# Kernel tuning notes

Measured on AMD Instinct MI355X. Metric: run time of the kernel, lower is better.

Reference implementation:

```python
import math
import jax, jax.numpy as jnp
import numpy as np

B, S, D, H = 1, 4096, 1024, 16
HD = D // H


def setup_inputs() -> dict:
    key = jax.random.key(0)
    ks = jax.random.split(key, 11)
    s = 0.02
    inp = {
        "q": jax.random.normal(ks[0], (B, S, D), jnp.float32),
        "k": jax.random.normal(ks[1], (B, S, D), jnp.float32),
        "v": jax.random.normal(ks[2], (B, S, D), jnp.float32),
        # causal boolean mask, broadcastable over [B, H, S, S]
        "mask": jnp.tril(jnp.ones((S, S), jnp.bool_))[None, None],
        "Wq": jax.random.normal(ks[3], (D, D), jnp.float32) * s,
        "bq": jnp.zeros((D,), jnp.float32),
        "Wk": jax.random.normal(ks[4], (D, D), jnp.float32) * s,
        "bk": jnp.zeros((D,), jnp.float32),
        "Wv": jax.random.normal(ks[5], (D, D), jnp.float32) * s,
        "bv": jnp.zeros((D,), jnp.float32),
        "Wo": jax.random.normal(ks[6], (D, D), jnp.float32) * s,
        "bo": jnp.zeros((D,), jnp.float32),
    }
    return inp


def reference(q, k, v, mask, Wq, bq, Wk, bk, Wv, bv, Wo, bo):
    # projections (torch Linear: x @ W.T + b; here W is stored already transposed)
    qp = (q @ Wq + bq).reshape(B, S, H, HD)
    kp = (k @ Wk + bk).reshape(B, S, H, HD)
    vp = (v @ Wv + bv).reshape(B, S, H, HD)
    # scores: [B, H, S, S]
    scores = jnp.einsum("bqhd,bkhd->bhqk", qp, kp) / math.sqrt(HD)
    scores = jnp.where(mask, scores, -jnp.inf)
    attn = jax.nn.softmax(scores, axis=-1)
    # context: [B, H, S, HD] -> [B, S, D]
    ctx = jnp.einsum("bhqk,bkhd->bqhd", attn, vp).reshape(B, S, D)
    return ctx @ Wo + bo
```

## Files before the change

### kernel.cpp

```cpp
#include <hip/hip_runtime.h>
#include <hip/hip_bf16.h>


#define S_LEN 4096
#define D_DIM 1024
#define NHEAD 16
#define HDIM  64

typedef __hip_bfloat16 bf16;
typedef __attribute__((ext_vector_type(8))) short bf16x8v;
typedef __attribute__((ext_vector_type(4))) float f32x4;

#define MFMA16(a, b, c) __builtin_amdgcn_mfma_f32_16x16x32_bf16((a), (b), (c), 0, 0, 0)

__device__ __forceinline__ void async_cp16(const void* g, void* l) {
    __builtin_amdgcn_global_load_lds(
        (const __attribute__((address_space(1))) unsigned int*)g,
        (__attribute__((address_space(3))) unsigned int*)l, 16, 0, 0);
}

__global__ __launch_bounds__(256) void cvt_bf16_k(
    const float* __restrict__ x0, const float* __restrict__ x1,
    const float* __restrict__ x2,
    bf16* __restrict__ y0, bf16* __restrict__ y1, bf16* __restrict__ y2)
{
    const float* x = (blockIdx.z == 0) ? x0 : (blockIdx.z == 1) ? x1 : x2;
    bf16*       y = (blockIdx.z == 0) ? y0 : (blockIdx.z == 1) ? y1 : y2;
    const size_t i = ((size_t)blockIdx.x * 256 + threadIdx.x);
    const float4 v = ((const float4*)x)[i];
    union { bf16 h[4]; short4 s; } u;
    u.h[0] = __float2bfloat16(v.x);
    u.h[1] = __float2bfloat16(v.y);
    u.h[2] = __float2bfloat16(v.z);
    u.h[3] = __float2bfloat16(v.w);
    ((short4*)y)[i] = u.s;
}

__global__ __launch_bounds__(256) void transpose_cvt_k(
    const float* __restrict__ W0, const float* __restrict__ W1,
    const float* __restrict__ W2, const float* __restrict__ W3,
    bf16* __restrict__ T0, bf16* __restrict__ T1,
    bf16* __restrict__ T2, bf16* __restrict__ T3)
{
    const float* W = (blockIdx.z == 0) ? W0 : (blockIdx.z == 1) ? W1
                   : (blockIdx.z == 2) ? W2 : W3;
    bf16*       Wt = (blockIdx.z == 0) ? T0 : (blockIdx.z == 1) ? T1
                   : (blockIdx.z == 2) ? T2 : T3;
    __shared__ float t[32][33];
    const int bx = blockIdx.x << 5, by = blockIdx.y << 5;
    const int tx = threadIdx.x & 31, ty = threadIdx.x >> 5;
#pragma unroll
    for (int i = 0; i < 32; i += 8)
        t[ty + i][tx] = W[(size_t)(by + ty + i) * D_DIM + bx + tx];
    __syncthreads();
#pragma unroll
    for (int i = 0; i < 32; i += 8)
        Wt[(size_t)(bx + ty + i) * D_DIM + by + tx] = __float2bfloat16(t[tx][ty + i]);
}

struct GemmJob {
    const bf16* A; const bf16* Wt; const float* bias; void* out;
    int mode; float scale;
};

__global__ __launch_bounds__(256) void gemm_k(GemmJob j0, GemmJob j1, GemmJob j2)
{
    const GemmJob j = (blockIdx.z == 0) ? j0 : (blockIdx.z == 1) ? j1 : j2;
    const int K = D_DIM;
    const int bn = blockIdx.x << 6;
    const int bm = blockIdx.y << 7;
    const int tid = threadIdx.x;
    const int w = tid >> 6, lane = tid & 63;
    const int col = lane & 15, g = lane >> 4;
    const int wr = (w >> 1) << 6, wc = (w & 1) << 5;

    __shared__ bf16 As[128 * 64];
    __shared__ bf16 Bs[64 * 64];

    f32x4 acc[4][2];
#pragma unroll
    for (int i = 0; i < 4; ++i)
#pragma unroll
        for (int jj = 0; jj < 2; ++jj) acc[i][jj] = (f32x4){0.f, 0.f, 0.f, 0.f};

    for (int kb = 0; kb < K; kb += 64) {
        __syncthreads();
#pragma unroll
        for (int e = 0; e < 4; ++e) {
            const int lin = (e << 8) + tid;
            const int row = lin >> 3, kc = lin & 7;
            async_cp16(j.A + (size_t)(bm + row) * K + kb + (kc << 3), &As[lin << 3]);
        }
#pragma unroll
        for (int e = 0; e < 2; ++e) {
            const int lin = (e << 8) + tid;
            const int row = lin >> 3, kc = lin & 7;
            async_cp16(j.Wt + (size_t)(bn + row) * K + kb + (kc << 3), &Bs[lin << 3]);
        }
        __syncthreads();

#pragma unroll
        for (int s = 0; s < 2; ++s) {
            bf16x8v af[4], bfv[2];
#pragma unroll
            for (int i = 0; i < 4; ++i)
                af[i] = *(const bf16x8v*)&As[((wr + (i << 4) + col) << 6) + (s << 5) + (g << 3)];
#pragma unroll
            for (int jj = 0; jj < 2; ++jj)
                bfv[jj] = *(const bf16x8v*)&Bs[((wc + (jj << 4) + col) << 6) + (s << 5) + (g << 3)];
#pragma unroll
            for (int i = 0; i < 4; ++i)
#pragma unroll
                for (int jj = 0; jj < 2; ++jj)
                    acc[i][jj] = MFMA16(af[i], bfv[jj], acc[i][jj]);
        }
    }

#pragma unroll
    for (int i = 0; i < 4; ++i)
#pragma unroll
    for (int jj = 0; jj < 2; ++jj)
#pragma unroll
    for (int reg = 0; reg < 4; ++reg) {
        const int row = bm + wr + (i << 4) + (g << 2) + reg;
        const int cg  = bn + wc + (jj << 4) + col;
        const float vv = (acc[i][jj][reg] + j.bias[cg]) * j.scale;
        if (j.mode == 0)
            ((bf16*)j.out)[(((size_t)(cg >> 6)) * S_LEN + row) * HDIM + (cg & 63)] =
                __float2bfloat16(vv);
        else if (j.mode == 2)
            ((bf16*)j.out)[((size_t)(cg >> 6) * HDIM + (cg & 63)) * S_LEN + row] =
                __float2bfloat16(vv);
        else
            ((float*)j.out)[(size_t)row * D_DIM + cg] = vv;
    }
}

__global__ __launch_bounds__(256) void attn_mfma_k(
    const bf16* __restrict__ Qp, const bf16* __restrict__ Kp,
    const bf16* __restrict__ Vt, bf16* __restrict__ ctx)
{
    __shared__ bf16 Ks[4096];
    __shared__ bf16 Vs[4096];
    __shared__ bf16 Ps[4][1024];

    const int bid = blockIdx.x;
    const int qb  = 63 - (bid >> 4);
    const int h   = bid & 15;
    const int q0  = qb << 6;
    const int tid = threadIdx.x, w = tid >> 6, lane = tid & 63;
    const int col = lane & 15, g = lane >> 4;

    const bf16* Kh = Kp + (size_t)h * S_LEN * HDIM;
    const bf16* Vh = Vt + (size_t)h * HDIM * S_LEN;

    const size_t qrow_base = ((size_t)h * S_LEN + q0 + (w << 4) + col) * HDIM + (g << 3);
    const bf16x8v qf0 = *(const bf16x8v*)(Qp + qrow_base);
    const bf16x8v qf1 = *(const bf16x8v*)(Qp + qrow_base + 32);

    const int sig_r = (col >> 2) | (((col & 3) ^ (g & 1)) << 2);
    const int pr0 = (((g) << 4) | sig_r) << 3;
    const int pr1 = (((4 + g) << 4) | sig_r) << 3;
    int pw[4][4];
#pragma unroll
    for (int t = 0; t < 4; ++t) {
        const int Gw = (t << 1) + (col >> 3);
#pragma unroll
        for (int reg = 0; reg < 4; ++reg) {
            const int sig = g | (((reg ^ (Gw & 1)) & 3) << 2);
            pw[t][reg] = (((Gw << 4) | sig) << 3) + (col & 7);
        }
    }

    float pl[4] = {0.f, 0.f, 0.f, 0.f};
    f32x4 acco[4];
#pragma unroll
    for (int t = 0; t < 4; ++t) acco[t] = (f32x4){0.f, 0.f, 0.f, 0.f};

    const int nkb = qb + 1;
    for (int kb = 0; kb < nkb; ++kb) {
        const int kk0 = kb << 6;
        __syncthreads();
#pragma unroll
        for (int e = 0; e < 2; ++e) {
            const int lin = (e << 8) + tid;
            const int t = lin >> 7, G = (lin >> 4) & 7, c = lin & 15;
            async_cp16(Kh + (size_t)(kk0 + (t << 4) + c) * HDIM + (G << 3),
                       &Ks[lin << 3]);
            async_cp16(Vh + (size_t)((t << 4) + c) * S_LEN + kk0 + (G << 3),
                       &Vs[lin << 3]);
        }
        __syncthreads();

        f32x4 sa[4];
#pragma unroll
        for (int t = 0; t < 4; ++t) sa[t] = (f32x4){0.f, 0.f, 0.f, 0.f};
#pragma unroll
        for (int t = 0; t < 4; ++t) {
            sa[t] = MFMA16(qf0, *(const bf16x8v*)&Ks[((t << 7) + (g << 4) + col) << 3], sa[t]);
            sa[t] = MFMA16(qf1, *(const bf16x8v*)&Ks[((t << 7) + 64 + (g << 4) + col) << 3], sa[t]);
        }

        const bool lastt = (kb == nkb - 1);
#pragma unroll
        for (int t = 0; t < 4; ++t) {
#pragma unroll
            for (int reg = 0; reg < 4; ++reg) {
                float p;
                if (lastt && (kk0 + (t << 4) + col > q0 + (w << 4) + (g << 2) + reg))
                    p = 0.f;
                else
                    p = __expf(sa[t][reg]);
                pl[reg] += p;
                Ps[w][pw[t][reg]] = __float2bfloat16(p);
            }
        }

        const bf16x8v pf0 = *(const bf16x8v*)&Ps[w][pr0];
        const bf16x8v pf1 = *(const bf16x8v*)&Ps[w][pr1];
#pragma unroll
        for (int t = 0; t < 4; ++t) {
            acco[t] = MFMA16(pf0, *(const bf16x8v*)&Vs[((t << 7) + (g << 4) + col) << 3], acco[t]);
            acco[t] = MFMA16(pf1, *(const bf16x8v*)&Vs[((t << 7) + 64 + (g << 4) + col) << 3], acco[t]);
        }
    }

    float lrow[4];
#pragma unroll
    for (int reg = 0; reg < 4; ++reg) {
        float l = pl[reg];
        l += __shfl_xor(l, 1);
        l += __shfl_xor(l, 2);
        l += __shfl_xor(l, 4);
        l += __shfl_xor(l, 8);
        lrow[reg] = l;
    }

#pragma unroll
    for (int t = 0; t < 4; ++t)
#pragma unroll
        for (int reg = 0; reg < 4; ++reg) {
            const int row = q0 + (w << 4) + (g << 2) + reg;
            ctx[(size_t)row * D_DIM + h * HDIM + (t << 4) + col] =
                __float2bfloat16(acco[t][reg] / lrow[reg]);
        }
}

extern "C" void kernel_launch(void* const* d_in, const int* in_sizes, int n_in,
                              void* d_out, int out_size, void* d_ws, size_t ws_size,
                              hipStream_t stream)
{
    const float* q  = (const float*)d_in[0];
    const float* k  = (const float*)d_in[1];
    const float* v  = (const float*)d_in[2];
    const float* Wq = (const float*)d_in[4];
    const float* bq = (const float*)d_in[5];
    const float* Wk = (const float*)d_in[6];
    const float* bk = (const float*)d_in[7];
    const float* Wv = (const float*)d_in[8];
    const float* bv = (const float*)d_in[9];
    const float* Wo = (const float*)d_in[10];
    const float* bo = (const float*)d_in[11];

    const size_t PE  = (size_t)S_LEN * D_DIM;
    const size_t WTE = (size_t)D_DIM * D_DIM;

    const dim3 tg(32, 32, 4);
    const dim3 gg(D_DIM / 64, S_LEN / 128, 1);
    const dim3 gg3(D_DIM / 64, S_LEN / 128, 3);
    const dim3 cg((unsigned)(PE / 1024), 1, 3);

    if (ws_size >= (size_t)64 * 1024 * 1024) {
        bf16* Qb = (bf16*)d_ws;
        bf16* Kb = Qb + PE;
        bf16* Vb = Kb + PE;
        bf16* Qp = Vb + PE;
        bf16* Kp = Qp + PE;
        bf16* Vt = Kp + PE;
        bf16* Wtq = Vt + PE;
        bf16* Wtk = Wtq + WTE;
        bf16* Wtv = Wtk + WTE;
        bf16* Wto = Wtv + WTE;
        bf16* ctx = Qb;

        transpose_cvt_k<<<tg, 256, 0, stream>>>(Wq, Wk, Wv, Wo, Wtq, Wtk, Wtv, Wto);
        cvt_bf16_k<<<cg, 256, 0, stream>>>(q, k, v, Qb, Kb, Vb);

        GemmJob jq{Qb, Wtq, bq, Qp, 0, 0.125f};
        GemmJob jk{Kb, Wtk, bk, Kp, 0, 1.0f};
        GemmJob jv{Vb, Wtv, bv, Vt, 2, 1.0f};
        gemm_k<<<gg3, 256, 0, stream>>>(jq, jk, jv);

        attn_mfma_k<<<dim3(1024), 256, 0, stream>>>(Qp, Kp, Vt, ctx);

        GemmJob jo{ctx, Wto, bo, d_out, 1, 1.0f};
        gemm_k<<<gg, 256, 0, stream>>>(jo, jo, jo);
    } else {
        bf16* X  = (bf16*)d_ws;
        bf16* Qp = X + PE;
        bf16* Kp = Qp + PE;
        bf16* Vt = Kp + PE;
        bf16* Wtq = Vt + PE;
        bf16* Wtk = Wtq + WTE;
        bf16* Wtv = Wtk + WTE;
        bf16* Wto = Wtv + WTE;

        transpose_cvt_k<<<tg, 256, 0, stream>>>(Wq, Wk, Wv, Wo, Wtq, Wtk, Wtv, Wto);

        const dim3 cg1((unsigned)(PE / 1024), 1, 1);
        cvt_bf16_k<<<cg1, 256, 0, stream>>>(q, q, q, X, X, X);
        GemmJob jq{X, Wtq, bq, Qp, 0, 0.125f};
        gemm_k<<<gg, 256, 0, stream>>>(jq, jq, jq);
        cvt_bf16_k<<<cg1, 256, 0, stream>>>(k, k, k, X, X, X);
        GemmJob jk{X, Wtk, bk, Kp, 0, 1.0f};
        gemm_k<<<gg, 256, 0, stream>>>(jk, jk, jk);
        cvt_bf16_k<<<cg1, 256, 0, stream>>>(v, v, v, X, X, X);
        GemmJob jv{X, Wtv, bv, Vt, 2, 1.0f};
        gemm_k<<<gg, 256, 0, stream>>>(jv, jv, jv);

        attn_mfma_k<<<dim3(1024), 256, 0, stream>>>(Qp, Kp, Vt, X);

        GemmJob jo{X, Wto, bo, d_out, 1, 1.0f};
        gemm_k<<<gg, 256, 0, stream>>>(jo, jo, jo);
    }
}
```

Baseline: 324.3 us.

## Restructure attention: 128-row query tiles, register P, register-prefetched K/V, XOR-swizzled LDS

The attention kernel now handles 128 query rows per block (two 16-row tiles per wave), so each K/V tile staged in shared memory is reused twice as often, and the grid shrinks to 512 blocks. It computes S transposed so the exp'd probabilities can be packed straight into MFMA operand registers, removing the per-wave shared-memory P round trip. Q is pre-scaled by log2(e) so exp2 can replace expf. The V projection output is written in a permuted row order to match the new P register layout, and the next K/V tile is prefetched into registers while the current one is computed. The GEMM shared-memory tiles also get an XOR swizzle to cut bank conflicts; in exchange there are more registers per thread, fewer blocks, and a tightly coupled layout between the GEMM and attention kernels.

After: 328.9 us. Within noise of the previous version (+1.4%).

```diff
diff --git a/kernel.cpp b/kernel.cpp
--- a/kernel.cpp
+++ b/kernel.cpp
@@ -12,11 +12,16 @@
 typedef __attribute__((ext_vector_type(4))) float f32x4;
 
 #define MFMA16(a, b, c) __builtin_amdgcn_mfma_f32_16x16x32_bf16((a), (b), (c), 0, 0, 0)
+#define LOG2E 1.44269504088896340736f
 
 __device__ __forceinline__ void async_cp16(const void* g, void* l) {
     __builtin_amdgcn_global_load_lds(
         (const __attribute__((address_space(1))) unsigned int*)g,
         (__attribute__((address_space(3))) unsigned int*)l, 16, 0, 0);
+}
+
+__device__ __forceinline__ short bf_bits(float x) {
+    union { bf16 h; short s; } u; u.h = __float2bfloat16(x); return u.s;
 }
 
 __global__ __launch_bounds__(256) void cvt_bf16_k(
@@ -88,14 +93,16 @@
 #pragma unroll
         for (int e = 0; e < 4; ++e) {
             const int lin = (e << 8) + tid;
-            const int row = lin >> 3, kc = lin & 7;
-            async_cp16(j.A + (size_t)(bm + row) * K + kb + (kc << 3), &As[lin << 3]);
+            const int row = lin >> 3, kcs = lin & 7;
+            const int kcg = kcs ^ (row & 7);
+            async_cp16(j.A + (size_t)(bm + row) * K + kb + (kcg << 3), &As[lin << 3]);
         }
 #pragma unroll
         for (int e = 0; e < 2; ++e) {
             const int lin = (e << 8) + tid;
-            const int row = lin >> 3, kc = lin & 7;
-            async_cp16(j.Wt + (size_t)(bn + row) * K + kb + (kc << 3), &Bs[lin << 3]);
+            const int row = lin >> 3, kcs = lin & 7;
+            const int kcg = kcs ^ (row & 7);
+            async_cp16(j.Wt + (size_t)(bn + row) * K + kb + (kcg << 3), &Bs[lin << 3]);
         }
         __syncthreads();
 
@@ -103,11 +110,15 @@
         for (int s = 0; s < 2; ++s) {
             bf16x8v af[4], bfv[2];
 #pragma unroll
-            for (int i = 0; i < 4; ++i)
-                af[i] = *(const bf16x8v*)&As[((wr + (i << 4) + col) << 6) + (s << 5) + (g << 3)];
-#pragma unroll
-            for (int jj = 0; jj < 2; ++jj)
-                bfv[jj] = *(const bf16x8v*)&Bs[((wc + (jj << 4) + col) << 6) + (s << 5) + (g << 3)];
+            for (int i = 0; i < 4; ++i) {
+                const int row = wr + (i << 4) + col;
+                af[i] = *(const bf16x8v*)&As[((row << 3) + (((s << 2) + g) ^ (row & 7))) << 3];
+            }
+#pragma unroll
+            for (int jj = 0; jj < 2; ++jj) {
+                const int row = wc + (jj << 4) + col;
+                bfv[jj] = *(const bf16x8v*)&Bs[((row << 3) + (((s << 2) + g) ^ (row & 7))) << 3];
+            }
 #pragma unroll
             for (int i = 0; i < 4; ++i)
 #pragma unroll
@@ -128,122 +139,172 @@
         if (j.mode == 0)
             ((bf16*)j.out)[(((size_t)(cg >> 6)) * S_LEN + row) * HDIM + (cg & 63)] =
                 __float2bfloat16(vv);
-        else if (j.mode == 2)
-            ((bf16*)j.out)[((size_t)(cg >> 6) * HDIM + (cg & 63)) * S_LEN + row] =
+        else if (j.mode == 2) {
+            const int lr = row & 63;
+            const int prow = (row & ~63) | (lr & 32)
+                           | (((lr & 15) >> 2) << 3)
+                           | ((lr & 3) + (((lr >> 4) & 1) << 2));
+            ((bf16*)j.out)[((size_t)(cg >> 6) * HDIM + (cg & 63)) * S_LEN + prow] =
                 __float2bfloat16(vv);
-        else
+        } else
             ((float*)j.out)[(size_t)row * D_DIM + cg] = vv;
     }
 }
 
 __global__ __launch_bounds__(256) void attn_mfma_k(
     const bf16* __restrict__ Qp, const bf16* __restrict__ Kp,
-    const bf16* __restrict__ Vt, bf16* __restrict__ ctx)
+    const bf16* __restrict__ Vtm, bf16* __restrict__ ctx)
 {
     __shared__ bf16 Ks[4096];
     __shared__ bf16 Vs[4096];
-    __shared__ bf16 Ps[4][1024];
 
     const int bid = blockIdx.x;
-    const int qb  = 63 - (bid >> 4);
+    const int qb  = 31 - (bid >> 4);
     const int h   = bid & 15;
-    const int q0  = qb << 6;
+    const int q0  = qb << 7;
+    const int nkb = (qb << 1) + 2;
     const int tid = threadIdx.x, w = tid >> 6, lane = tid & 63;
     const int col = lane & 15, g = lane >> 4;
 
-    const bf16* Kh = Kp + (size_t)h * S_LEN * HDIM;
-    const bf16* Vh = Vt + (size_t)h * HDIM * S_LEN;
-
-    const size_t qrow_base = ((size_t)h * S_LEN + q0 + (w << 4) + col) * HDIM + (g << 3);
-    const bf16x8v qf0 = *(const bf16x8v*)(Qp + qrow_base);
-    const bf16x8v qf1 = *(const bf16x8v*)(Qp + qrow_base + 32);
-
-    const int sig_r = (col >> 2) | (((col & 3) ^ (g & 1)) << 2);
-    const int pr0 = (((g) << 4) | sig_r) << 3;
-    const int pr1 = (((4 + g) << 4) | sig_r) << 3;
-    int pw[4][4];
-#pragma unroll
-    for (int t = 0; t < 4; ++t) {
-        const int Gw = (t << 1) + (col >> 3);
+    const bf16* Kh = Kp  + (size_t)h * S_LEN * HDIM;
+    const bf16* Vh = Vtm + (size_t)h * HDIM * S_LEN;
+
+    bf16x8v qf[2][2];
+#pragma unroll
+    for (int u = 0; u < 2; ++u) {
+        const size_t qrb = ((size_t)h * S_LEN + q0 + (w << 5) + (u << 4) + col) * HDIM + (g << 3);
+        qf[u][0] = *(const bf16x8v*)(Qp + qrb);
+        qf[u][1] = *(const bf16x8v*)(Qp + qrb + 32);
+    }
+
+    const int L0 = tid, L1 = 256 + tid;
+    const int k0r = L0 >> 3, k0G = L0 & 7;
+    const int k1r = L1 >> 3, k1G = L1 & 7;
+    const int sl0 = ((k0r >> 4) << 7) + (k0G << 4) + ((k0r & 15) ^ k0G);
+    const int sl1 = ((k1r >> 4) << 7) + (k1G << 4) + ((k1r & 15) ^ k1G);
+    const size_t v0base = (size_t)k0r * S_LEN + (k0G << 3);
+    const size_t v1base = (size_t)k1r * S_LEN + (k1G << 3);
+
+    float pl[2] = {0.f, 0.f};
+    f32x4 acco[2][4];
+#pragma unroll
+    for (int u = 0; u < 2; ++u)
+#pragma unroll
+        for (int t = 0; t < 4; ++t) acco[u][t] = (f32x4){0.f, 0.f, 0.f, 0.f};
+
+    {
+        bf16x8v ka = *(const bf16x8v*)(Kh + ((size_t)L0 << 3));
+        bf16x8v kb_ = *(const bf16x8v*)(Kh + ((size_t)L1 << 3));
+        bf16x8v va = *(const bf16x8v*)(Vh + v0base);
+        bf16x8v vb = *(const bf16x8v*)(Vh + v1base);
+        *(bf16x8v*)&Ks[sl0 << 3] = ka;
+        *(bf16x8v*)&Ks[sl1 << 3] = kb_;
+        *(bf16x8v*)&Vs[sl0 << 3] = va;
+        *(bf16x8v*)&Vs[sl1 << 3] = vb;
+    }
+    __syncthreads();
+
+    for (int kb = 0; kb < nkb; ++kb) {
+        bf16x8v kn0, kn1, vn0, vn1;
+        const bool more = (kb + 1 < nkb);
+        if (more) {
+            const size_t kbase = (size_t)(kb + 1) << 12;
+            kn0 = *(const bf16x8v*)(Kh + kbase + ((size_t)L0 << 3));
+            kn1 = *(const bf16x8v*)(Kh + kbase + ((size_t)L1 << 3));
+            const int koff = (kb + 1) << 6;
+            vn0 = *(const bf16x8v*)(Vh + v0base + koff);
+            vn1 = *(const bf16x8v*)(Vh + v1base + koff);
+        }
+
+        f32x4 sa[2][4];
+#pragma unroll
+        for (int u = 0; u < 2; ++u)
+#pragma unroll
+            for (int t = 0; t < 4; ++t) sa[u][t] = (f32x4){0.f, 0.f, 0.f, 0.f};
+#pragma unroll
+        for (int t = 0; t < 4; ++t) {
+            const int G0 = g, G1 = 4 + g;
+            const bf16x8v kf0 = *(const bf16x8v*)&Ks[(((t << 7) + (G0 << 4) + (col ^ G0))) << 3];
+            const bf16x8v kf1 = *(const bf16x8v*)&Ks[(((t << 7) + (G1 << 4) + (col ^ G1))) << 3];
+            sa[0][t] = MFMA16(kf0, qf[0][0], sa[0][t]);
+            sa[0][t] = MFMA16(kf1, qf[0][1], sa[0][t]);
+            sa[1][t] = MFMA16(kf0, qf[1][0], sa[1][t]);
+            sa[1][t] = MFMA16(kf1, qf[1][1], sa[1][t]);
+        }
+
+        bf16x8v pf[2][2];
+        const bool maskzone = (kb + 2 >= nkb);
+#pragma unroll
+        for (int u = 0; u < 2; ++u) {
+            float ps[4][4];
+            if (!maskzone) {
+#pragma unroll
+                for (int t = 0; t < 4; ++t)
+#pragma unroll
+                    for (int reg = 0; reg < 4; ++reg)
+                        ps[t][reg] = __builtin_amdgcn_exp2f(sa[u][t][reg]);
+            } else {
+                const int qrel = q0 + (w << 5) + (u << 4) + col - (kb << 6);
+#pragma unroll
+                for (int t = 0; t < 4; ++t)
+#pragma unroll
+                    for (int reg = 0; reg < 4; ++reg) {
+                        const int krel = (t << 4) + (g << 2) + reg;
+                        ps[t][reg] = (krel > qrel) ? 0.f
+                                   : __builtin_amdgcn_exp2f(sa[u][t][reg]);
+                    }
+            }
+#pragma unroll
+            for (int t = 0; t < 4; ++t)
+                pl[u] += (ps[t][0] + ps[t][1]) + (ps[t][2] + ps[t][3]);
+            bf16x8v a, b;
+#pragma unroll
+            for (int reg = 0; reg < 4; ++reg) {
+                a[reg]     = bf_bits(ps[0][reg]);
+                a[4 + reg] = bf_bits(ps[1][reg]);
+                b[reg]     = bf_bits(ps[2][reg]);
+                b[4 + reg] = bf_bits(ps[3][reg]);
+            }
+            pf[u][0] = a; pf[u][1] = b;
+        }
+
+#pragma unroll
+        for (int t = 0; t < 4; ++t) {
+            const int G0 = g, G1 = 4 + g;
+            const bf16x8v vf0 = *(const bf16x8v*)&Vs[(((t << 7) + (G0 << 4) + (col ^ G0))) << 3];
+            const bf16x8v vf1 = *(const bf16x8v*)&Vs[(((t << 7) + (G1 << 4) + (col ^ G1))) << 3];
+            acco[0][t] = MFMA16(pf[0][0], vf0, acco[0][t]);
+            acco[0][t] = MFMA16(pf[0][1], vf1, acco[0][t]);
+            acco[1][t] = MFMA16(pf[1][0], vf0, acco[1][t]);
+            acco[1][t] = MFMA16(pf[1][1], vf1, acco[1][t]);
+        }
+
+        if (more) {
+            __syncthreads();
+            *(bf16x8v*)&Ks[sl0 << 3] = kn0;
+            *(bf16x8v*)&Ks[sl1 << 3] = kn1;
+            *(bf16x8v*)&Vs[sl0 << 3] = vn0;
+            *(bf16x8v*)&Vs[sl1 << 3] = vn1;
+            __syncthreads();
+        }
+    }
+
+#pragma unroll
+    for (int u = 0; u < 2; ++u) {
+        float l = pl[u];
+        l += __shfl_xor(l, 16);
+        l += __shfl_xor(l, 32);
 #pragma unroll
         for (int reg = 0; reg < 4; ++reg) {
-            const int sig = g | (((reg ^ (Gw & 1)) & 3) << 2);
-            pw[t][reg] = (((Gw << 4) | sig) << 3) + (col & 7);
-        }
-    }
-
-    float pl[4] = {0.f, 0.f, 0.f, 0.f};
-    f32x4 acco[4];
-#pragma unroll
-    for (int t = 0; t < 4; ++t) acco[t] = (f32x4){0.f, 0.f, 0.f, 0.f};
-
-    const int nkb = qb + 1;
-    for (int kb = 0; kb < nkb; ++kb) {
-        const int kk0 = kb << 6;
-        __syncthreads();
-#pragma unroll
-        for (int e = 0; e < 2; ++e) {
-            const int lin = (e << 8) + tid;
-            const int t = lin >> 7, G = (lin >> 4) & 7, c = lin & 15;
-            async_cp16(Kh + (size_t)(kk0 + (t << 4) + c) * HDIM + (G << 3),
-                       &Ks[lin << 3]);
-            async_cp16(Vh + (size_t)((t << 4) + c) * S_LEN + kk0 + (G << 3),
-                       &Vs[lin << 3]);
-        }
-        __syncthreads();
-
-        f32x4 sa[4];
-#pragma unroll
-        for (int t = 0; t < 4; ++t) sa[t] = (f32x4){0.f, 0.f, 0.f, 0.f};
-#pragma unroll
-        for (int t = 0; t < 4; ++t) {
-            sa[t] = MFMA16(qf0, *(const bf16x8v*)&Ks[((t << 7) + (g << 4) + col) << 3], sa[t]);
-            sa[t] = MFMA16(qf1, *(const bf16x8v*)&Ks[((t << 7) + 64 + (g << 4) + col) << 3], sa[t]);
-        }
-
-        const bool lastt = (kb == nkb - 1);
-#pragma unroll
-        for (int t = 0; t < 4; ++t) {
-#pragma unroll
-            for (int reg = 0; reg < 4; ++reg) {
-                float p;
-                if (lastt && (kk0 + (t << 4) + col > q0 + (w << 4) + (g << 2) + reg))
-                    p = 0.f;
-                else
-                    p = __expf(sa[t][reg]);
-                pl[reg] += p;
-                Ps[w][pw[t][reg]] = __float2bfloat16(p);
-            }
-        }
-
-        const bf16x8v pf0 = *(const bf16x8v*)&Ps[w][pr0];
-        const bf16x8v pf1 = *(const bf16x8v*)&Ps[w][pr1];
-#pragma unroll
-        for (int t = 0; t < 4; ++t) {
-            acco[t] = MFMA16(pf0, *(const bf16x8v*)&Vs[((t << 7) + (g << 4) + col) << 3], acco[t]);
-            acco[t] = MFMA16(pf1, *(const bf16x8v*)&Vs[((t << 7) + 64 + (g << 4) + col) << 3], acco[t]);
-        }
-    }
-
-    float lrow[4];
-#pragma unroll
-    for (int reg = 0; reg < 4; ++reg) {
-        float l = pl[reg];
-        l += __shfl_xor(l, 1);
-        l += __shfl_xor(l, 2);
-        l += __shfl_xor(l, 4);
-        l += __shfl_xor(l, 8);
-        lrow[reg] = l;
-    }
-
-#pragma unroll
-    for (int t = 0; t < 4; ++t)
-#pragma unroll
-        for (int reg = 0; reg < 4; ++reg) {
-            const int row = q0 + (w << 4) + (g << 2) + reg;
-            ctx[(size_t)row * D_DIM + h * HDIM + (t << 4) + col] =
-                __float2bfloat16(acco[t][reg] / lrow[reg]);
-        }
+            const float lr = __shfl(l, (g << 2) + reg);
+#pragma unroll
+            for (int t = 0; t < 4; ++t) {
+                const int row = q0 + (w << 5) + (u << 4) + (g << 2) + reg;
+                ctx[(size_t)row * D_DIM + h * HDIM + (t << 4) + col] =
+                    __float2bfloat16(acco[u][t][reg] / lr);
+            }
+        }
+    }
 }
 
 extern "C" void kernel_launch(void* const* d_in, const int* in_sizes, int n_in,
@@ -264,6 +325,7 @@
 
     const size_t PE  = (size_t)S_LEN * D_DIM;
     const size_t WTE = (size_t)D_DIM * D_DIM;
+    const float qscale = 0.125f * LOG2E;
 
     const dim3 tg(32, 32, 4);
     const dim3 gg(D_DIM / 64, S_LEN / 128, 1);
@@ -286,12 +348,12 @@
         transpose_cvt_k<<<tg, 256, 0, stream>>>(Wq, Wk, Wv, Wo, Wtq, Wtk, Wtv, Wto);
         cvt_bf16_k<<<cg, 256, 0, stream>>>(q, k, v, Qb, Kb, Vb);
 
-        GemmJob jq{Qb, Wtq, bq, Qp, 0, 0.125f};
+        GemmJob jq{Qb, Wtq, bq, Qp, 0, qscale};
         GemmJob jk{Kb, Wtk, bk, Kp, 0, 1.0f};
         GemmJob jv{Vb, Wtv, bv, Vt, 2, 1.0f};
         gemm_k<<<gg3, 256, 0, stream>>>(jq, jk, jv);
 
-        attn_mfma_k<<<dim3(1024), 256, 0, stream>>>(Qp, Kp, Vt, ctx);
+        attn_mfma_k<<<dim3(512), 256, 0, stream>>>(Qp, Kp, Vt, ctx);
 
         GemmJob jo{ctx, Wto, bo, d_out, 1, 1.0f};
         gemm_k<<<gg, 256, 0, stream>>>(jo, jo, jo);
@@ -309,7 +371,7 @@
 
         const dim3 cg1((unsigned)(PE / 1024), 1, 1);
         cvt_bf16_k<<<cg1, 256, 0, stream>>>(q, q, q, X, X, X);
-        GemmJob jq{X, Wtq, bq, Qp, 0, 0.125f};
+        GemmJob jq{X, Wtq, bq, Qp, 0, qscale};
         gemm_k<<<gg, 256, 0, stream>>>(jq, jq, jq);
         cvt_bf16_k<<<cg1, 256, 0, stream>>>(k, k, k, X, X, X);
         GemmJob jk{X, Wtk, bk, Kp, 0, 1.0f};
@@ -318,7 +380,7 @@
         GemmJob jv{X, Wtv, bv, Vt, 2, 1.0f};
         gemm_k<<<gg, 256, 0, stream>>>(jv, jv, jv);
 
-        attn_mfma_k<<<dim3(1024), 256, 0, stream>>>(Qp, Kp, Vt, X);
+        attn_mfma_k<<<dim3(512), 256, 0, stream>>>(Qp, Kp, Vt, X);
 
         GemmJob jo{X, Wto, bo, d_out, 1, 1.0f};
         gemm_k<<<gg, 256, 0, stream>>>(jo, jo, jo);
```
